# Kernel optimization log

Hardware: AMD Instinct MI355X
Metric: run time of the kernel (lower is better)

The kernel has to match this reference:

```python
import jax, jax.numpy as jnp
import numpy as np

B, LE, LD = 8, 4096, 4096
DE, DD, A = 512, 512, 128


def setup_inputs() -> dict:
    key = jax.random.key(0)
    ks = jax.random.split(key, 9)
    f32 = jnp.float32
    return {
        "encoder_outputs": jax.random.normal(ks[0], (B, LE, DE), f32),
        "decoder_outputs": jax.random.normal(ks[1], (B, LD, DD), f32),
        # linear_q / linear_k / linear_v (Dense with bias, relu activation)
        "Wq": jax.random.normal(ks[2], (DD, A), f32) * 0.05,
        "bq": jnp.zeros((A,), f32),
        "Wk": jax.random.normal(ks[3], (DE, A), f32) * 0.05,
        "bk": jnp.zeros((A,), f32),
        "Wv": jax.random.normal(ks[4], (DE, A), f32) * 0.05,
        "bv": jnp.zeros((A,), f32),
        # perceptron branch weights (Dense, no bias)
        "Pw": jax.random.normal(ks[5], (A, A), f32) * 0.05,
        "Pu": jax.random.normal(ks[6], (A, A), f32) * 0.05,
        "pv": jax.random.normal(ks[7], (A, 1), f32) * 0.05,
    }


def reference(encoder_outputs, decoder_outputs, Wq, bq, Wk, bk, Wv, bv, Pw, Pu, pv):
    att = Wq.shape[1]
    q = jax.nn.relu(decoder_outputs @ Wq + bq)   # [B, Ld, A]
    k = jax.nn.relu(encoder_outputs @ Wk + bk)   # [B, Le, A]
    v = jax.nn.relu(encoder_outputs @ Wv + bv)   # [B, Le, A]
    # perceptron score: pv^T (Pw q_i + Pu k_j). No nonlinearity between the
    # sum and pv, so it decomposes additively -> no [B,Ld,Le,A] tiling needed.
    q_term = (q @ Pw) @ pv                        # [B, Ld, 1]
    k_term = (k @ Pu) @ pv                        # [B, Le, 1]
    scores = (q_term + jnp.swapaxes(k_term, 1, 2)) / jnp.sqrt(jnp.float32(att))  # [B, Ld, Le]
    weights = jax.nn.softmax(scores, axis=-1)
    attention = jnp.einsum('bij,bjd->bid', weights, v)  # [B, Ld, A]
    return attention
```

## Files before the change

kernel.cpp:

```cpp
#include <hip/hip_runtime.h>
#include <hip/hip_bf16.h>

#define B_   8
#define KDIM 512
#define AA_  128
#define RTOT 32768
#define BM   64
#define NGRID (RTOT/BM)

typedef __attribute__((ext_vector_type(8))) short short8;
typedef __attribute__((ext_vector_type(4))) float f32x4;

#define WCT_OFF   0
#define U_OFF     262144
#define BIAS_OFF  262656
#define PARTS_OFF 263680
#define S_OFF     394752
#define VB_OFF    525824

__device__ inline ushort f2bf(float f) {
    union { float f; unsigned u; } x; x.f = f;
    unsigned r = x.u + 0x7fffu + ((x.u >> 16) & 1u);
    return (ushort)(r >> 16);
}
__device__ inline float bf2f(ushort s) {
    union { unsigned u; float f; } x; x.u = ((unsigned)s) << 16;
    return x.f;
}

__device__ __forceinline__ void glds16(const void* g, void* l) {
    __builtin_amdgcn_global_load_lds(
        (const __attribute__((address_space(1))) void*)g,
        (__attribute__((address_space(3))) void*)l, 16, 0, 0);
}

__global__ void prep_kernel(const float* __restrict__ Wk, const float* __restrict__ bk,
                            const float* __restrict__ Wv, const float* __restrict__ bv,
                            const float* __restrict__ Pu, const float* __restrict__ pv,
                            ushort* __restrict__ wct, float* __restrict__ u,
                            float* __restrict__ bias) {
    int t = threadIdx.x;
    int base = blockIdx.x * 256 + t;
    for (int i = 0; i < 4; ++i) {
        int idx = base + i * 32768;
        int n = idx >> 9, kdst = idx & 511;
        int st = kdst >> 6, s = (kdst >> 3) & 7, e = kdst & 7;
        int j = s ^ (n & 7);
        int ksrc = st * 64 + j * 8 + e;
        float v = (n < 128) ? Wk[ksrc * 128 + n] : Wv[ksrc * 128 + (n - 128)];
        wct[idx] = f2bf(v);
    }
    if (blockIdx.x == 0) {
        if (t < 128) {
            float acc = 0.f;
            for (int c = 0; c < 128; ++c) acc += Pu[t * 128 + c] * pv[c];
            u[t] = acc;
        }
        bias[t] = (t < 128) ? bk[t] : bv[t - 128];
    }
}

__global__ __launch_bounds__(256, 2)
void gemm_fused(const float* __restrict__ enc, const ushort* __restrict__ wct,
                const float* __restrict__ bias, const float* __restrict__ u,
                ushort* __restrict__ vbuf, float* __restrict__ sout) {
    __shared__ ushort Bs[2][256 * 64];
    __shared__ ushort As[BM][72];
    __shared__ float s_red[BM][2];
    const int t = threadIdx.x;
    const int wv = t >> 6, l = t & 63;
    const int m = l & 15, kb = l >> 4;
    const int row0 = blockIdx.x * BM;

    const int ar0 = t >> 3, ak8 = (t & 7) * 8;
    const float* ap0 = enc + (size_t)(row0 + ar0) * KDIM + ak8;
    const float* ap1 = ap0 + (size_t)32 * KDIM;

    const char* wct_c = (const char*)wct;

    f32x4 acc[4][4] = {};
    float4 a0, a1, a2, a3;

    a0 = *(const float4*)ap0; a1 = *(const float4*)(ap0 + 4);
    a2 = *(const float4*)ap1; a3 = *(const float4*)(ap1 + 4);
#pragma unroll
    for (int i = 0; i < 8; ++i) {
        int c = (wv << 3) | i;
        int row = (c << 3) + (l >> 3);
        glds16(wct_c + (size_t)row * 1024 + ((l & 7) << 4),
               (char*)&Bs[0][0] + c * 1024 + l * 16);
    }

#pragma unroll
    for (int st = 0; st < 8; ++st) {
        const int bufc = st & 1;
        {
            int4 pk;
            pk.x = (int)f2bf(a0.x) | ((int)f2bf(a0.y) << 16);
            pk.y = (int)f2bf(a0.z) | ((int)f2bf(a0.w) << 16);
            pk.z = (int)f2bf(a1.x) | ((int)f2bf(a1.y) << 16);
            pk.w = (int)f2bf(a1.z) | ((int)f2bf(a1.w) << 16);
            *(int4*)&As[ar0][ak8] = pk;
            pk.x = (int)f2bf(a2.x) | ((int)f2bf(a2.y) << 16);
            pk.y = (int)f2bf(a2.z) | ((int)f2bf(a2.w) << 16);
            pk.z = (int)f2bf(a3.x) | ((int)f2bf(a3.y) << 16);
            pk.w = (int)f2bf(a3.z) | ((int)f2bf(a3.w) << 16);
            *(int4*)&As[ar0 + 32][ak8] = pk;
        }
        if (st < 7) {
            const float* p0 = ap0 + (st + 1) * 64;
            const float* p1 = ap1 + (st + 1) * 64;
            a0 = *(const float4*)p0; a1 = *(const float4*)(p0 + 4);
            a2 = *(const float4*)p1; a3 = *(const float4*)(p1 + 4);
            const char* gb = wct_c + (size_t)(st + 1) * 128;
#pragma unroll
            for (int i = 0; i < 8; ++i) {
                int c = (wv << 3) | i;
                int row = (c << 3) + (l >> 3);
                glds16(gb + (size_t)row * 1024 + ((l & 7) << 4),
                       (char*)&Bs[bufc ^ 1][0] + c * 1024 + l * 16);
            }
            asm volatile("s_waitcnt vmcnt(12) lgkmcnt(0)" ::: "memory");
        } else {
            asm volatile("s_waitcnt vmcnt(0) lgkmcnt(0)" ::: "memory");
        }
        __builtin_amdgcn_sched_barrier(0);
        __builtin_amdgcn_s_barrier();
#pragma unroll
        for (int kc = 0; kc < 2; ++kc) {
            short8 afr[4], bfr[4];
#pragma unroll
            for (int mt = 0; mt < 4; ++mt)
                afr[mt] = *(const short8*)&As[mt * 16 + m][kc * 32 + kb * 8];
#pragma unroll
            for (int nt = 0; nt < 4; ++nt) {
                int r = wv * 64 + nt * 16 + m;
                int s = (kc * 4 + kb) ^ (r & 7);
                bfr[nt] = *(const short8*)&Bs[bufc][r * 64 + s * 8];
            }
#pragma unroll
            for (int mt = 0; mt < 4; ++mt)
#pragma unroll
                for (int nt = 0; nt < 4; ++nt)
                    acc[mt][nt] = __builtin_amdgcn_mfma_f32_16x16x32_bf16(
                        afr[mt], bfr[nt], acc[mt][nt], 0, 0, 0);
        }
        asm volatile("" ::: "memory");
        __builtin_amdgcn_s_barrier();
    }

    const int rg = kb;
    if (wv < 2) {
#pragma unroll
        for (int mt = 0; mt < 4; ++mt) {
            float p[4] = {0.f, 0.f, 0.f, 0.f};
#pragma unroll
            for (int nt = 0; nt < 4; ++nt) {
                int col = wv * 64 + nt * 16 + m;
                float bsv = bias[col], uw = u[col];
#pragma unroll
                for (int j = 0; j < 4; ++j) {
                    float vvv = acc[mt][nt][j] + bsv;
                    vvv = vvv > 0.f ? vvv : 0.f;
                    p[j] += vvv * uw;
                }
            }
#pragma unroll
            for (int j = 0; j < 4; ++j) {
                p[j] += __shfl_xor(p[j], 1);
                p[j] += __shfl_xor(p[j], 2);
                p[j] += __shfl_xor(p[j], 4);
                p[j] += __shfl_xor(p[j], 8);
            }
            if (m == 0) {
#pragma unroll
                for (int j = 0; j < 4; ++j)
                    s_red[mt * 16 + rg * 4 + j][wv] = p[j];
            }
        }
    } else {
#pragma unroll
        for (int mt = 0; mt < 4; ++mt) {
#pragma unroll
            for (int nt = 0; nt < 4; ++nt) {
                int col = wv * 64 + nt * 16 + m;
                float bsv = bias[col];
#pragma unroll
                for (int j = 0; j < 4; ++j) {
                    int rowl = mt * 16 + rg * 4 + j;
                    float vvv = acc[mt][nt][j] + bsv;
                    vvv = vvv > 0.f ? vvv : 0.f;
                    vbuf[(size_t)(row0 + rowl) * AA_ + (col - 128)] = f2bf(vvv);
                }
            }
        }
    }
    __syncthreads();
    if (t < BM) sout[row0 + t] = s_red[t][0] + s_red[t][1];
}

__global__ __launch_bounds__(256)
void wsum_kernel(const ushort* __restrict__ vbuf, const float* __restrict__ sg,
                 float* __restrict__ parts) {
    __shared__ float redM[5], redS[5];
    __shared__ float pw[4][128];
    const int blk = blockIdx.x;
    const int b = blk >> 5, ch = blk & 31;
    const int t = threadIdx.x, wv = t >> 6, l = t & 63;
    const float inv_s = 0.08838834764831843f;

    float vl[16], mx = -1e30f;
#pragma unroll
    for (int i = 0; i < 16; ++i) {
        vl[i] = sg[b * 4096 + i * 256 + t];
        mx = fmaxf(mx, vl[i]);
    }
#pragma unroll
    for (int off = 1; off < 64; off <<= 1) mx = fmaxf(mx, __shfl_xor(mx, off));
    if (l == 0) redM[wv] = mx;
    __syncthreads();
    if (t == 0) redM[4] = fmaxf(fmaxf(redM[0], redM[1]), fmaxf(redM[2], redM[3]));
    __syncthreads();
    const float M = redM[4];
    float sm = 0.f;
#pragma unroll
    for (int i = 0; i < 16; ++i) sm += __expf((vl[i] - M) * inv_s);
#pragma unroll
    for (int off = 1; off < 64; off <<= 1) sm += __shfl_xor(sm, off);
    if (l == 0) redS[wv] = sm;
    __syncthreads();
    if (t == 0) redS[4] = 1.0f / (redS[0] + redS[1] + redS[2] + redS[3]);
    __syncthreads();
    const float rS = redS[4];

    const int rg = l >> 4, d8 = (l & 15) * 8;
    const int rbase = b * 4096 + ch * 128;
    float acc[8] = {};
#pragma unroll
    for (int it = 0; it < 8; ++it) {
        int r = rbase + it * 16 + wv * 4 + rg;
        float wj = __expf((sg[r] - M) * inv_s) * rS;
        short8 vvv = *(const short8*)(vbuf + (size_t)r * AA_ + d8);
#pragma unroll
        for (int j = 0; j < 8; ++j)
            acc[j] += wj * bf2f((ushort)vvv[j]);
    }
#pragma unroll
    for (int j = 0; j < 8; ++j) {
        acc[j] += __shfl_xor(acc[j], 16);
        acc[j] += __shfl_xor(acc[j], 32);
    }
    if (l < 16) {
#pragma unroll
        for (int j = 0; j < 8; ++j) pw[wv][d8 + j] = acc[j];
    }
    __syncthreads();
    if (t < 128) parts[blk * 128 + t] = pw[0][t] + pw[1][t] + pw[2][t] + pw[3][t];
}

__global__ __launch_bounds__(256)
void bcast_kernel(const float* __restrict__ parts, float4* __restrict__ out) {
    __shared__ float redp[2][128];
    __shared__ float nvf[128];
    const int t = threadIdx.x;
    const int b = blockIdx.x >> 7;
    const int d = t & 127, h = t >> 7;
    float s = 0.f;
#pragma unroll
    for (int i = 0; i < 16; ++i)
        s += parts[(size_t)(b * 32 + h * 16 + i) * 128 + d];
    redp[h][d] = s;
    __syncthreads();
    if (t < 128) nvf[t] = redp[0][t] + redp[1][t];
    __syncthreads();
    const float4 val = ((const float4*)nvf)[t & 31];
    float4* o4 = out + (size_t)blockIdx.x * 1024;
#pragma unroll
    for (int it = 0; it < 4; ++it)
        o4[it * 256 + t] = val;
}

extern "C" void kernel_launch(void* const* d_in, const int* in_sizes, int n_in,
                              void* d_out, int out_size, void* d_ws, size_t ws_size,
                              hipStream_t stream) {
    const float* enc = (const float*)d_in[0];
    const float* Wk = (const float*)d_in[4];
    const float* bk = (const float*)d_in[5];
    const float* Wv = (const float*)d_in[6];
    const float* bv = (const float*)d_in[7];
    const float* Pu = (const float*)d_in[9];
    const float* pv = (const float*)d_in[10];

    char* ws = (char*)d_ws;
    ushort* wct   = (ushort*)(ws + WCT_OFF);
    float*  u     = (float*)(ws + U_OFF);
    float*  bias  = (float*)(ws + BIAS_OFF);
    float*  parts = (float*)(ws + PARTS_OFF);
    float*  sg    = (float*)(ws + S_OFF);
    ushort* vbuf  = (ushort*)(ws + VB_OFF);

    prep_kernel<<<128, 256, 0, stream>>>(Wk, bk, Wv, bv, Pu, pv, wct, u, bias);
    gemm_fused<<<NGRID, 256, 0, stream>>>(enc, wct, bias, u, vbuf, sg);
    wsum_kernel<<<256, 256, 0, stream>>>(vbuf, sg, parts);
    bcast_kernel<<<1024, 256, 0, stream>>>(parts, (float4*)d_out);
}
```

Measured before the change: 177.3 us.

## Compute softmax exponent in GEMM epilogue and accumulate sums via atomics

```diff
diff --git a/kernel.cpp b/kernel.cpp
--- a/kernel.cpp
+++ b/kernel.cpp
@@ -14,9 +14,10 @@
 #define WCT_OFF   0
 #define U_OFF     262144
 #define BIAS_OFF  262656
-#define PARTS_OFF 263680
-#define S_OFF     394752
-#define VB_OFF    525824
+#define NUM_OFF   263680
+#define SB_OFF    267776
+#define S_OFF     267840
+#define VB_OFF    398912
 
 __device__ inline ushort f2bf(float f) {
     union { float f; unsigned u; } x; x.f = f;
@@ -38,7 +39,8 @@
                             const float* __restrict__ Wv, const float* __restrict__ bv,
                             const float* __restrict__ Pu, const float* __restrict__ pv,
                             ushort* __restrict__ wct, float* __restrict__ u,
-                            float* __restrict__ bias) {
+                            float* __restrict__ bias, float* __restrict__ num,
+                            float* __restrict__ Sb) {
     int t = threadIdx.x;
     int base = blockIdx.x * 256 + t;
     for (int i = 0; i < 4; ++i) {
@@ -57,13 +59,16 @@
             u[t] = acc;
         }
         bias[t] = (t < 128) ? bk[t] : bv[t - 128];
+        for (int i = 0; i < 4; ++i) num[t + i * 256] = 0.f;
+        if (t < 8) Sb[t] = 0.f;
     }
 }
 
 __global__ __launch_bounds__(256, 2)
 void gemm_fused(const float* __restrict__ enc, const ushort* __restrict__ wct,
                 const float* __restrict__ bias, const float* __restrict__ u,
-                ushort* __restrict__ vbuf, float* __restrict__ sout) {
+                ushort* __restrict__ vbuf, float* __restrict__ sout,
+                float* __restrict__ Sb) {
     __shared__ ushort Bs[2][256 * 64];
     __shared__ ushort As[BM][72];
     __shared__ float s_red[BM][2];
@@ -196,42 +201,25 @@
         }
     }
     __syncthreads();
-    if (t < BM) sout[row0 + t] = s_red[t][0] + s_red[t][1];
+    if (t < BM) {
+        const float inv_s = 0.08838834764831843f;
+        float e = __expf((s_red[t][0] + s_red[t][1]) * inv_s);
+        sout[row0 + t] = e;
+        float tot = e;
+#pragma unroll
+        for (int off = 1; off < 64; off <<= 1) tot += __shfl_xor(tot, off);
+        if (t == 0) atomicAdd(&Sb[row0 >> 12], tot);
+    }
 }
 
 __global__ __launch_bounds__(256)
 void wsum_kernel(const ushort* __restrict__ vbuf, const float* __restrict__ sg,
-                 float* __restrict__ parts) {
-    __shared__ float redM[5], redS[5];
+                 const float* __restrict__ Sb, float* __restrict__ num) {
     __shared__ float pw[4][128];
     const int blk = blockIdx.x;
     const int b = blk >> 5, ch = blk & 31;
     const int t = threadIdx.x, wv = t >> 6, l = t & 63;
-    const float inv_s = 0.08838834764831843f;
-
-    float vl[16], mx = -1e30f;
-#pragma unroll
-    for (int i = 0; i < 16; ++i) {
-        vl[i] = sg[b * 4096 + i * 256 + t];
-        mx = fmaxf(mx, vl[i]);
-    }
-#pragma unroll
-    for (int off = 1; off < 64; off <<= 1) mx = fmaxf(mx, __shfl_xor(mx, off));
-    if (l == 0) redM[wv] = mx;
-    __syncthreads();
-    if (t == 0) redM[4] = fmaxf(fmaxf(redM[0], redM[1]), fmaxf(redM[2], redM[3]));
-    __syncthreads();
-    const float M = redM[4];
-    float sm = 0.f;
-#pragma unroll
-    for (int i = 0; i < 16; ++i) sm += __expf((vl[i] - M) * inv_s);
-#pragma unroll
-    for (int off = 1; off < 64; off <<= 1) sm += __shfl_xor(sm, off);
-    if (l == 0) redS[wv] = sm;
-    __syncthreads();
-    if (t == 0) redS[4] = 1.0f / (redS[0] + redS[1] + redS[2] + redS[3]);
-    __syncthreads();
-    const float rS = redS[4];
+    const float rS = 1.0f / Sb[b];
 
     const int rg = l >> 4, d8 = (l & 15) * 8;
     const int rbase = b * 4096 + ch * 128;
@@ -239,7 +227,7 @@
 #pragma unroll
     for (int it = 0; it < 8; ++it) {
         int r = rbase + it * 16 + wv * 4 + rg;
-        float wj = __expf((sg[r] - M) * inv_s) * rS;
+        float wj = sg[r] * rS;
         short8 vvv = *(const short8*)(vbuf + (size_t)r * AA_ + d8);
 #pragma unroll
         for (int j = 0; j < 8; ++j)
@@ -255,25 +243,18 @@
         for (int j = 0; j < 8; ++j) pw[wv][d8 + j] = acc[j];
     }
     __syncthreads();
-    if (t < 128) parts[blk * 128 + t] = pw[0][t] + pw[1][t] + pw[2][t] + pw[3][t];
+    if (t < 128)
+        atomicAdd(&num[b * 128 + t], pw[0][t] + pw[1][t] + pw[2][t] + pw[3][t]);
 }
 
 __global__ __launch_bounds__(256)
-void bcast_kernel(const float* __restrict__ parts, float4* __restrict__ out) {
-    __shared__ float redp[2][128];
-    __shared__ float nvf[128];
+void bcast_kernel(const float* __restrict__ num, float4* __restrict__ out) {
+    __shared__ float4 nv[32];
     const int t = threadIdx.x;
     const int b = blockIdx.x >> 7;
-    const int d = t & 127, h = t >> 7;
-    float s = 0.f;
-#pragma unroll
-    for (int i = 0; i < 16; ++i)
-        s += parts[(size_t)(b * 32 + h * 16 + i) * 128 + d];
-    redp[h][d] = s;
+    if (t < 32) nv[t] = ((const float4*)(num + b * 128))[t];
     __syncthreads();
-    if (t < 128) nvf[t] = redp[0][t] + redp[1][t];
-    __syncthreads();
-    const float4 val = ((const float4*)nvf)[t & 31];
+    const float4 val = nv[t & 31];
     float4* o4 = out + (size_t)blockIdx.x * 1024;
 #pragma unroll
     for (int it = 0; it < 4; ++it)
@@ -295,12 +276,13 @@
     ushort* wct   = (ushort*)(ws + WCT_OFF);
     float*  u     = (float*)(ws + U_OFF);
     float*  bias  = (float*)(ws + BIAS_OFF);
-    float*  parts = (float*)(ws + PARTS_OFF);
+    float*  num   = (float*)(ws + NUM_OFF);
+    float*  Sb    = (float*)(ws + SB_OFF);
     float*  sg    = (float*)(ws + S_OFF);
     ushort* vbuf  = (ushort*)(ws + VB_OFF);
 
-    prep_kernel<<<128, 256, 0, stream>>>(Wk, bk, Wv, bv, Pu, pv, wct, u, bias);
-    gemm_fused<<<NGRID, 256, 0, stream>>>(enc, wct, bias, u, vbuf, sg);
-    wsum_kernel<<<256, 256, 0, stream>>>(vbuf, sg, parts);
-    bcast_kernel<<<1024, 256, 0, stream>>>(parts, (float4*)d_out);
-}
+    prep_kernel<<<128, 256, 0, stream>>>(Wk, bk, Wv, bv, Pu, pv, wct, u, bias, num, Sb);
+    gemm_fused<<<NGRID, 256, 0, stream>>>(enc, wct, bias, u, vbuf, sg, Sb);
+    wsum_kernel<<<256, 256, 0, stream>>>(vbuf, sg, Sb, num);
+    bcast_kernel<<<1024, 256, 0, stream>>>(num, (float4*)d_out);
+}
```

Measured after the change: 179.9 us. No clear change (+1.5%).
